# Optimization experiments

Measured on AMD Instinct MI355X. Metric: run time of the kernel, lower is better.

The kernel has to match this reference:

```python
import jax, jax.numpy as jnp
import numpy as np

RESOLUTION = 2 ** 8  # 256
N_POINTS = 2 ** 21


def setup_inputs() -> dict:
    key = jax.random.key(0)
    k1, k2 = jax.random.split(key)
    inp = jax.random.uniform(k1, (N_POINTS, 3), dtype=jnp.float32)
    grid = jax.random.normal(k2, (RESOLUTION, RESOLUTION, RESOLUTION, 3), dtype=jnp.float32) * 0.01
    return {"input": inp, "feature_params": grid}


def reference(input, feature_params):
    R = feature_params.shape[0]
    scaled = input * (R - 1)
    lower = jnp.clip(jnp.floor(scaled).astype(jnp.int32), 0, R - 2)
    upper = jnp.clip(lower + 1, 0, R - 1)
    t = scaled - lower.astype(scaled.dtype)
    xl, yl, zl = lower[:, 0], lower[:, 1], lower[:, 2]
    xu, yu, zu = upper[:, 0], upper[:, 1], upper[:, 2]
    tx, ty, tz = t[:, 0:1], t[:, 1:2], t[:, 2:3]  # (N,1) for broadcast over channels
    # note original indexes grid as [z, y, x]
    c000 = feature_params[zl, yl, xl]
    c001 = feature_params[zl, yl, xu]
    c010 = feature_params[zl, yu, xl]
    c011 = feature_params[zl, yu, xu]
    c100 = feature_params[zu, yl, xl]
    c101 = feature_params[zu, yl, xu]
    c110 = feature_params[zu, yu, xl]
    c111 = feature_params[zu, yu, xu]
    c00 = c000 * (1 - tx) + c001 * tx
    c01 = c010 * (1 - tx) + c011 * tx
    c10 = c100 * (1 - tx) + c101 * tx
    c11 = c110 * (1 - tx) + c111 * tx
    c0 = c00 * (1 - ty) + c01 * ty
    c1 = c10 * (1 - ty) + c11 * ty
    return c0 * (1 - tz) + c1 * tz
```

## Files before the change

kernel.cpp:

```cpp
#include <hip/hip_runtime.h>


#define NB     4096
#define GBLK   512
#define CHUNKF 196
#define NCHUNK 81
#define NF4    (NCHUNK * 49)
#define LDSF   (NF4 * 4)

#define OFF_OFF   33554432u
#define CUR_OFF   (33554432u + 16388u)
#define HIST_OFF  (33554432u + 16388u + 16384u)
#define NEEDED    (33554432u + 65536u)

typedef float f4v __attribute__((ext_vector_type(4)));
typedef float f2v __attribute__((ext_vector_type(2)));
typedef f4v f4u __attribute__((aligned(8)));
typedef f2v f2u __attribute__((aligned(8)));

__device__ __forceinline__ void cell_of(float p, int& l, float& t) {
    float s = p * 255.0f;
    int v = (int)floorf(s);
    v = v < 0 ? 0 : (v > 254 ? 254 : v);
    l = v;
    t = s - (float)v;
}

__device__ __forceinline__ int fine_bin3(float px, float py, float pz) {
    int xl, yl, zl; float tx, ty, tz;
    cell_of(px, xl, tx);
    cell_of(py, yl, ty);
    cell_of(pz, zl, tz);
    return ((((zl >> 3) << 5) | (yl >> 3)) << 2) | (xl >> 6);
}

__global__ __launch_bounds__(1024) void k_hist(const float* __restrict__ inp,
                                               unsigned* __restrict__ hist, int n) {
    __shared__ unsigned h[NB];
    int t = threadIdx.x;
    for (int i = t; i < NB; i += 1024) h[i] = 0;
    __syncthreads();
    int stride = gridDim.x * 1024;
    for (int i = blockIdx.x * 1024 + t; i < n; i += stride)
        atomicAdd(&h[fine_bin3(inp[3 * i], inp[3 * i + 1], inp[3 * i + 2])], 1u);
    __syncthreads();
    for (int i = t; i < NB; i += 1024)
        if (h[i]) atomicAdd(&hist[i], h[i]);
}

__global__ __launch_bounds__(1024) void k_scan(const unsigned* __restrict__ hist,
                                               unsigned* __restrict__ off,
                                               unsigned* __restrict__ cur) {
    __shared__ unsigned s[1024];
    int t = threadIdx.x;
    unsigned v0 = hist[4 * t], v1 = hist[4 * t + 1];
    unsigned v2 = hist[4 * t + 2], v3 = hist[4 * t + 3];
    unsigned sum = v0 + v1 + v2 + v3;
    s[t] = sum;
    __syncthreads();
    for (int d = 1; d < 1024; d <<= 1) {
        unsigned add = (t >= d) ? s[t - d] : 0u;
        __syncthreads();
        s[t] += add;
        __syncthreads();
    }
    unsigned excl = s[t] - sum;
    unsigned e0 = excl, e1 = excl + v0, e2 = e1 + v1, e3 = e2 + v2;
    off[4 * t] = e0;     cur[4 * t] = e0;
    off[4 * t + 1] = e1; cur[4 * t + 1] = e1;
    off[4 * t + 2] = e2; cur[4 * t + 2] = e2;
    off[4 * t + 3] = e3; cur[4 * t + 3] = e3;
    if (t == 1023) off[NB] = s[1023];
}

__global__ __launch_bounds__(1024) void k_scatter(const float* __restrict__ inp,
                                                  float4* __restrict__ binned,
                                                  unsigned* __restrict__ cur, int n) {
    __shared__ unsigned cnt[NB];
    __shared__ unsigned base[NB];
    int t = threadIdx.x;
    int stride = gridDim.x * 1024;
    int iters = (n + stride - 1) / stride;
    for (int it = 0; it < iters; ++it) {
        int i = it * stride + blockIdx.x * 1024 + t;
        for (int k = t; k < NB; k += 1024) cnt[k] = 0;
        __syncthreads();
        int b = 0; unsigned r = 0; float px = 0, py = 0, pz = 0;
        bool valid = (i < n);
        if (valid) {
            px = inp[3 * i];
            py = inp[3 * i + 1];
            pz = inp[3 * i + 2];
            b = fine_bin3(px, py, pz);
            r = atomicAdd(&cnt[b], 1u);
        }
        __syncthreads();
        for (int k = t; k < NB; k += 1024)
            if (cnt[k]) base[k] = atomicAdd(&cur[k], cnt[k]);
        __syncthreads();
        if (valid) {
            float4 v;
            v.x = px; v.y = py; v.z = pz; v.w = __uint_as_float((unsigned)i);
            binned[base[b] + r] = v;
        }
        __syncthreads();
    }
}

__global__ __launch_bounds__(GBLK) void k_gather(const float4* __restrict__ binned,
                                                 const float* __restrict__ grid,
                                                 const unsigned* __restrict__ off,
                                                 float* __restrict__ out) {
    __shared__ __align__(16) float slab[LDSF];
    int bin = blockIdx.x;
    int x0 = (bin & 3) << 6;
    int y0 = ((bin >> 2) & 31) << 3;
    int z0 = (bin >> 7) << 3;
    int t = threadIdx.x;

    unsigned start = off[bin], end = off[bin + 1];
    unsigned count = end - start;

    float4 v;
    if ((unsigned)t < count) v = binned[start + (unsigned)t];

    for (int u0 = 0; u0 < NF4; u0 += GBLK) {
        int u = u0 + t;
        if (u < NF4) {
            int chunk = u / 49;
            int j = u - chunk * 49;
            int zc = chunk / 9;
            int yc = chunk - zc * 9;
            int zg = z0 + zc; zg = zg > 255 ? 255 : zg;
            int yg = y0 + yc; yg = yg > 255 ? 255 : yg;
            int joff = (j == 48 && x0 == 192) ? 0 : (j << 2);
            const float* src = grid + (size_t)((zg << 16) | (yg << 8) | x0) * 3 + joff;
            __builtin_amdgcn_global_load_lds(
                (const __attribute__((address_space(1))) unsigned int*)src,
                (__attribute__((address_space(3))) unsigned int*)&slab[(size_t)u * 4],
                16, 0, 0);
        }
    }
    __syncthreads();

    unsigned p = (unsigned)t;
    while (p < count) {
        float px = v.x, py = v.y, pz = v.z;
        unsigned idx = __float_as_uint(v.w);
        p += (unsigned)GBLK;
        if (p < count) v = binned[start + p];

        int xl, yl, zl; float tx, ty, tz;
        cell_of(px, xl, tx);
        cell_of(py, yl, ty);
        cell_of(pz, zl, tz);
        int xc = xl - x0, yc = yl - y0, zc = zl - z0;

        int r0 = (zc * 9 + yc) * CHUNKF + xc * 3;
        int e = r0 & ~1;
        bool d = (r0 & 1) != 0;

#define SEG_READ(b, s)                                   \
        do {                                             \
            f2v q0 = *(const f2u*)(&slab[(b)]);          \
            f2v q1 = *(const f2u*)(&slab[(b) + 2]);      \
            f2v q2 = *(const f2u*)(&slab[(b) + 4]);      \
            f2v q3 = *(const f2u*)(&slab[(b) + 6]);      \
            s[0] = d ? q0.y : q0.x;                      \
            s[1] = d ? q1.x : q0.y;                      \
            s[2] = d ? q1.y : q1.x;                      \
            s[3] = d ? q2.x : q1.y;                      \
            s[4] = d ? q2.y : q2.x;                      \
            s[5] = d ? q3.x : q2.y;                      \
        } while (0)

        float s00[6], s01[6], s10[6], s11[6];
        SEG_READ(e,               s00);
        SEG_READ(e + CHUNKF,      s01);
        SEG_READ(e + 9 * CHUNKF,  s10);
        SEG_READ(e + 10 * CHUNKF, s11);
#undef SEG_READ

        float o[3];
#pragma unroll
        for (int c = 0; c < 3; ++c) {
            float c00 = s00[c] * (1.0f - tx) + s00[c + 3] * tx;
            float c01 = s01[c] * (1.0f - tx) + s01[c + 3] * tx;
            float c10 = s10[c] * (1.0f - tx) + s10[c + 3] * tx;
            float c11 = s11[c] * (1.0f - tx) + s11[c + 3] * tx;
            float c0 = c00 * (1.0f - ty) + c01 * ty;
            float c1 = c10 * (1.0f - ty) + c11 * ty;
            o[c] = c0 * (1.0f - tz) + c1 * tz;
        }
        float3 w; w.x = o[0]; w.y = o[1]; w.z = o[2];
        *(float3*)(out + 3 * (size_t)idx) = w;
    }
}

__global__ __launch_bounds__(256) void k_direct(const float* __restrict__ inp,
                                                const float* __restrict__ grid,
                                                float* __restrict__ out, int n) {
    int i = blockIdx.x * blockDim.x + threadIdx.x;
    if (i >= n) return;
    int xl, yl, zl; float tx, ty, tz;
    cell_of(inp[3 * i + 0], xl, tx);
    cell_of(inp[3 * i + 1], yl, ty);
    cell_of(inp[3 * i + 2], zl, tz);
    int b00 = (zl * 65536 + yl * 256 + xl) * 3;
    int b01 = b00 + 768, b10 = b00 + 196608, b11 = b10 + 768;
    float s00[6], s01[6], s10[6], s11[6];
#pragma unroll
    for (int kk = 0; kk < 6; ++kk) s00[kk] = grid[b00 + kk];
#pragma unroll
    for (int kk = 0; kk < 6; ++kk) s01[kk] = grid[b01 + kk];
#pragma unroll
    for (int kk = 0; kk < 6; ++kk) s10[kk] = grid[b10 + kk];
#pragma unroll
    for (int kk = 0; kk < 6; ++kk) s11[kk] = grid[b11 + kk];
#pragma unroll
    for (int c = 0; c < 3; ++c) {
        float c00 = s00[c] * (1.0f - tx) + s00[c + 3] * tx;
        float c01 = s01[c] * (1.0f - tx) + s01[c + 3] * tx;
        float c10 = s10[c] * (1.0f - tx) + s10[c + 3] * tx;
        float c11 = s11[c] * (1.0f - tx) + s11[c + 3] * tx;
        float c0 = c00 * (1.0f - ty) + c01 * ty;
        float c1 = c10 * (1.0f - ty) + c11 * ty;
        out[3 * i + c] = c0 * (1.0f - tz) + c1 * tz;
    }
}

extern "C" void kernel_launch(void* const* d_in, const int* in_sizes, int n_in,
                              void* d_out, int out_size, void* d_ws, size_t ws_size,
                              hipStream_t stream) {
    const float* inp  = (const float*)d_in[0];
    const float* grid = (const float*)d_in[1];
    float* out = (float*)d_out;
    int n = in_sizes[0] / 3;

    if (ws_size < (size_t)NEEDED) {
        int blocks = (n + 255) / 256;
        k_direct<<<blocks, 256, 0, stream>>>(inp, grid, out, n);
        return;
    }

    char* ws = (char*)d_ws;
    float4*   binned = (float4*)ws;
    unsigned* off    = (unsigned*)(ws + OFF_OFF);
    unsigned* cur    = (unsigned*)(ws + CUR_OFF);
    unsigned* hist   = (unsigned*)(ws + HIST_OFF);

    hipMemsetAsync(hist, 0, NB * sizeof(unsigned), stream);
    k_hist   <<<256, 1024, 0, stream>>>(inp, hist, n);
    k_scan   <<<1,   1024, 0, stream>>>(hist, off, cur);
    k_scatter<<<256, 1024, 0, stream>>>(inp, binned, cur, n);
    k_gather <<<NB,  GBLK, 0, stream>>>(binned, grid, off, out);
}
```

Measured before the change: 157.7 us.

## Halve gather bin width, vectorize point loads, replace memset with zero kernel

```diff
diff --git a/kernel.cpp b/kernel.cpp
--- a/kernel.cpp
+++ b/kernel.cpp
@@ -1,17 +1,17 @@
 #include <hip/hip_runtime.h>
 
 
-#define NB     4096
+#define NB     8192
 #define GBLK   512
-#define CHUNKF 196
+#define CHUNKF 100
 #define NCHUNK 81
-#define NF4    (NCHUNK * 49)
-#define LDSF   (NF4 * 4)
+#define NF4    2025
+#define LDSF   8100
 
 #define OFF_OFF   33554432u
-#define CUR_OFF   (33554432u + 16388u)
-#define HIST_OFF  (33554432u + 16388u + 16384u)
-#define NEEDED    (33554432u + 65536u)
+#define CUR_OFF   (33554432u + 32772u)
+#define HIST_OFF  (33554432u + 32772u + 32768u)
+#define NEEDED    (33554432u + 32772u + 32768u + 32768u)
 
 typedef float f4v __attribute__((ext_vector_type(4)));
 typedef float f2v __attribute__((ext_vector_type(2)));
@@ -31,7 +31,12 @@
     cell_of(px, xl, tx);
     cell_of(py, yl, ty);
     cell_of(pz, zl, tz);
-    return ((((zl >> 3) << 5) | (yl >> 3)) << 2) | (xl >> 6);
+    return ((zl >> 3) << 8) | ((yl >> 3) << 3) | (xl >> 5);
+}
+
+__global__ __launch_bounds__(1024) void k_zero(unsigned* __restrict__ hist) {
+    int i = blockIdx.x * 1024 + threadIdx.x;
+    if (i < NB) hist[i] = 0;
 }
 
 __global__ __launch_bounds__(1024) void k_hist(const float* __restrict__ inp,
@@ -40,9 +45,18 @@
     int t = threadIdx.x;
     for (int i = t; i < NB; i += 1024) h[i] = 0;
     __syncthreads();
+    int P = n >> 1;
     int stride = gridDim.x * 1024;
-    for (int i = blockIdx.x * 1024 + t; i < n; i += stride)
-        atomicAdd(&h[fine_bin3(inp[3 * i], inp[3 * i + 1], inp[3 * i + 2])], 1u);
+    for (int pr = blockIdx.x * 1024 + t; pr < P; pr += stride) {
+        f4v a = *(const f4u*)(inp + 6 * pr);
+        f2v b = *(const f2u*)(inp + 6 * pr + 4);
+        atomicAdd(&h[fine_bin3(a.x, a.y, a.z)], 1u);
+        atomicAdd(&h[fine_bin3(a.w, b.x, b.y)], 1u);
+    }
+    if ((n & 1) && blockIdx.x == 0 && t == 0) {
+        int i = n - 1;
+        atomicAdd(&hist[fine_bin3(inp[3 * i], inp[3 * i + 1], inp[3 * i + 2])], 1u);
+    }
     __syncthreads();
     for (int i = t; i < NB; i += 1024)
         if (h[i]) atomicAdd(&hist[i], h[i]);
@@ -53,9 +67,10 @@
                                                unsigned* __restrict__ cur) {
     __shared__ unsigned s[1024];
     int t = threadIdx.x;
-    unsigned v0 = hist[4 * t], v1 = hist[4 * t + 1];
-    unsigned v2 = hist[4 * t + 2], v3 = hist[4 * t + 3];
-    unsigned sum = v0 + v1 + v2 + v3;
+    unsigned v[8];
+    unsigned sum = 0;
+#pragma unroll
+    for (int k = 0; k < 8; ++k) { v[k] = hist[8 * t + k]; sum += v[k]; }
     s[t] = sum;
     __syncthreads();
     for (int d = 1; d < 1024; d <<= 1) {
@@ -64,12 +79,13 @@
         s[t] += add;
         __syncthreads();
     }
-    unsigned excl = s[t] - sum;
-    unsigned e0 = excl, e1 = excl + v0, e2 = e1 + v1, e3 = e2 + v2;
-    off[4 * t] = e0;     cur[4 * t] = e0;
-    off[4 * t + 1] = e1; cur[4 * t + 1] = e1;
-    off[4 * t + 2] = e2; cur[4 * t + 2] = e2;
-    off[4 * t + 3] = e3; cur[4 * t + 3] = e3;
+    unsigned e = s[t] - sum;
+#pragma unroll
+    for (int k = 0; k < 8; ++k) {
+        off[8 * t + k] = e;
+        cur[8 * t + k] = e;
+        e += v[k];
+    }
     if (t == 1023) off[NB] = s[1023];
 }
 
@@ -79,43 +95,59 @@
     __shared__ unsigned cnt[NB];
     __shared__ unsigned base[NB];
     int t = threadIdx.x;
+    int P = n >> 1;
     int stride = gridDim.x * 1024;
-    int iters = (n + stride - 1) / stride;
+    int iters = (P + stride - 1) / stride;
+
+    if ((n & 1) && blockIdx.x == 0 && t == 0) {
+        int i = n - 1;
+        float px = inp[3 * i], py = inp[3 * i + 1], pz = inp[3 * i + 2];
+        int b = fine_bin3(px, py, pz);
+        unsigned r = atomicAdd(&cur[b], 1u);
+        float4 v; v.x = px; v.y = py; v.z = pz; v.w = __uint_as_float((unsigned)i);
+        binned[r] = v;
+    }
+
     for (int it = 0; it < iters; ++it) {
-        int i = it * stride + blockIdx.x * 1024 + t;
+        int pr = it * stride + blockIdx.x * 1024 + t;
         for (int k = t; k < NB; k += 1024) cnt[k] = 0;
         __syncthreads();
-        int b = 0; unsigned r = 0; float px = 0, py = 0, pz = 0;
-        bool valid = (i < n);
+        int b0 = 0, b1 = 0; unsigned r0 = 0, r1 = 0;
+        float4 p0, p1;
+        bool valid = (pr < P);
         if (valid) {
-            px = inp[3 * i];
-            py = inp[3 * i + 1];
-            pz = inp[3 * i + 2];
-            b = fine_bin3(px, py, pz);
-            r = atomicAdd(&cnt[b], 1u);
+            f4v a = *(const f4u*)(inp + 6 * pr);
+            f2v b = *(const f2u*)(inp + 6 * pr + 4);
+            p0.x = a.x; p0.y = a.y; p0.z = a.z;
+            p0.w = __uint_as_float((unsigned)(2 * pr));
+            p1.x = a.w; p1.y = b.x; p1.z = b.y;
+            p1.w = __uint_as_float((unsigned)(2 * pr + 1));
+            b0 = fine_bin3(p0.x, p0.y, p0.z);
+            b1 = fine_bin3(p1.x, p1.y, p1.z);
+            r0 = atomicAdd(&cnt[b0], 1u);
+            r1 = atomicAdd(&cnt[b1], 1u);
         }
         __syncthreads();
         for (int k = t; k < NB; k += 1024)
             if (cnt[k]) base[k] = atomicAdd(&cur[k], cnt[k]);
         __syncthreads();
         if (valid) {
-            float4 v;
-            v.x = px; v.y = py; v.z = pz; v.w = __uint_as_float((unsigned)i);
-            binned[base[b] + r] = v;
+            binned[base[b0] + r0] = p0;
+            binned[base[b1] + r1] = p1;
         }
         __syncthreads();
     }
 }
 
-__global__ __launch_bounds__(GBLK) void k_gather(const float4* __restrict__ binned,
-                                                 const float* __restrict__ grid,
-                                                 const unsigned* __restrict__ off,
-                                                 float* __restrict__ out) {
+__global__ __launch_bounds__(GBLK, 8) void k_gather(const float4* __restrict__ binned,
+                                                    const float* __restrict__ grid,
+                                                    const unsigned* __restrict__ off,
+                                                    float* __restrict__ out) {
     __shared__ __align__(16) float slab[LDSF];
     int bin = blockIdx.x;
-    int x0 = (bin & 3) << 6;
-    int y0 = ((bin >> 2) & 31) << 3;
-    int z0 = (bin >> 7) << 3;
+    int x0 = (bin & 7) << 5;
+    int y0 = ((bin >> 3) & 31) << 3;
+    int z0 = (bin >> 8) << 3;
     int t = threadIdx.x;
 
     unsigned start = off[bin], end = off[bin + 1];
@@ -124,22 +156,19 @@
     float4 v;
     if ((unsigned)t < count) v = binned[start + (unsigned)t];
 
-    for (int u0 = 0; u0 < NF4; u0 += GBLK) {
-        int u = u0 + t;
-        if (u < NF4) {
-            int chunk = u / 49;
-            int j = u - chunk * 49;
-            int zc = chunk / 9;
-            int yc = chunk - zc * 9;
-            int zg = z0 + zc; zg = zg > 255 ? 255 : zg;
-            int yg = y0 + yc; yg = yg > 255 ? 255 : yg;
-            int joff = (j == 48 && x0 == 192) ? 0 : (j << 2);
-            const float* src = grid + (size_t)((zg << 16) | (yg << 8) | x0) * 3 + joff;
-            __builtin_amdgcn_global_load_lds(
-                (const __attribute__((address_space(1))) unsigned int*)src,
-                (__attribute__((address_space(3))) unsigned int*)&slab[(size_t)u * 4],
-                16, 0, 0);
-        }
+    for (int u = t; u < NF4; u += GBLK) {
+        int chunk = u / 25;
+        int j = u - chunk * 25;
+        int zc = chunk / 9;
+        int yc = chunk - zc * 9;
+        int zg = z0 + zc; zg = zg > 255 ? 255 : zg;
+        int yg = y0 + yc; yg = yg > 255 ? 255 : yg;
+        int joff = (j == 24 && x0 == 224) ? 0 : (j << 2);
+        const float* src = grid + (size_t)((zg << 16) | (yg << 8) | x0) * 3 + joff;
+        __builtin_amdgcn_global_load_lds(
+            (const __attribute__((address_space(1))) unsigned int*)src,
+            (__attribute__((address_space(3))) unsigned int*)&slab[(size_t)u * 4],
+            16, 0, 0);
     }
     __syncthreads();
 
@@ -249,7 +278,7 @@
     unsigned* cur    = (unsigned*)(ws + CUR_OFF);
     unsigned* hist   = (unsigned*)(ws + HIST_OFF);
 
-    hipMemsetAsync(hist, 0, NB * sizeof(unsigned), stream);
+    k_zero   <<<8,   1024, 0, stream>>>(hist);
     k_hist   <<<256, 1024, 0, stream>>>(inp, hist, n);
     k_scan   <<<1,   1024, 0, stream>>>(hist, off, cur);
     k_scatter<<<256, 1024, 0, stream>>>(inp, binned, cur, n);
```

Measured after the change: 146.9 us. -6.9%, faster.
